# Kernel optimization log

Hardware: AMD Instinct MI355X
Metric: run time of the kernel (lower is better)

## Reference

```python
import jax, jax.numpy as jnp
import numpy as np

EMB = 1024
HEADS = 16
HEAD_DIM = EMB // HEADS
B, T = 2, 2048
EPS = 1e-5


def setup_inputs() -> dict:
    key = jax.random.key(0)
    ks = jax.random.split(key, 12)
    s_in = (1.0 / np.sqrt(EMB)).astype(np.float32)
    s_hid = (1.0 / np.sqrt(4 * EMB)).astype(np.float32)
    return {
        "x": jax.random.normal(ks[0], (B, T, EMB), jnp.float32),
        "Wq": jax.random.normal(ks[1], (HEADS, EMB, HEAD_DIM), jnp.float32) * s_in,
        "Wk": jax.random.normal(ks[2], (HEADS, EMB, HEAD_DIM), jnp.float32) * s_in,
        "Wv": jax.random.normal(ks[3], (HEADS, EMB, HEAD_DIM), jnp.float32) * s_in,
        "W1": jax.random.normal(ks[4], (EMB, 4 * EMB), jnp.float32) * s_in,
        "b1": jnp.zeros((4 * EMB,), jnp.float32),
        "W2": jax.random.normal(ks[5], (4 * EMB, EMB), jnp.float32) * s_hid,
        "b2": jnp.zeros((EMB,), jnp.float32),
        "g1": jnp.ones((EMB,), jnp.float32),
        "be1": jnp.zeros((EMB,), jnp.float32),
        "g2": jnp.ones((EMB,), jnp.float32),
        "be2": jnp.zeros((EMB,), jnp.float32),
    }


def _layernorm1d(x, gain, bias):
    # Faithful to source: normalize over dim 1 (sequence dim of [B,T,C]),
    # with UNBIASED variance (torch.var default).
    mean = jnp.mean(x, axis=1, keepdims=True)
    var = jnp.var(x, axis=1, keepdims=True, ddof=1)
    return gain * (x - mean) / jnp.sqrt(var + EPS) + bias


def _attention(x, Wq, Wk, Wv):
    Bq, Tq, C = x.shape
    q = jnp.einsum("btc,hcd->bhtd", x, Wq)
    k = jnp.einsum("btc,hcd->bhtd", x, Wk)
    v = jnp.einsum("btc,hcd->bhtd", x, Wv)
    # NOTE: scale uses input channel dim C (=emb_size), as in the source.
    wei = jnp.einsum("bhtd,bhsd->bhts", q, k) * (C ** -0.5)
    causal = jnp.tril(jnp.ones((Tq, Tq), bool))
    wei = jnp.where(causal, wei, -jnp.inf)
    wei = jax.nn.softmax(wei, axis=-1)
    out = jnp.einsum("bhts,bhsd->bhtd", wei, v)
    # concat over heads (dim=-1) == transpose + reshape
    return out.transpose(0, 2, 1, 3).reshape(Bq, Tq, -1)


def reference(x, Wq, Wk, Wv, W1, b1, W2, b2, g1, be1, g2, be2):
    x = x + _attention(_layernorm1d(x, g1, be1), Wq, Wk, Wv)
    h = _layernorm1d(x, g2, be2)
    h = jax.nn.relu(h @ W1 + b1) @ W2 + b2
    return x + h
```

## Files before the change

kernel.cpp:

```cpp
#include <hip/hip_runtime.h>


typedef __bf16 bf16x8 __attribute__((ext_vector_type(8)));
typedef float f32x4 __attribute__((ext_vector_type(4)));
typedef unsigned short u16;
typedef u16 u16x8 __attribute__((ext_vector_type(8)));
typedef u16 u16x4 __attribute__((ext_vector_type(4)));

#define MFMA16 __builtin_amdgcn_mfma_f32_16x16x32_bf16

__device__ __forceinline__ u16 f2bf(float f) {
  return __builtin_bit_cast(u16, (__bf16)f);
}
__device__ __forceinline__ float bf2f(u16 u) {
  return __builtin_bit_cast(float, (unsigned)u << 16);
}
__device__ __forceinline__ bf16x8 ldbf8(const u16* p) {
  return __builtin_bit_cast(bf16x8, *reinterpret_cast<const u16x8*>(p));
}
__device__ __forceinline__ void gll16(const void* g, void* l) {
  __builtin_amdgcn_global_load_lds((const __attribute__((address_space(1))) void*)g,
                                   (__attribute__((address_space(3))) void*)l, 16, 0, 0);
}
template <int N>
__device__ __forceinline__ void wait_vm() {
  if constexpr (N == 0)      asm volatile("s_waitcnt vmcnt(0)" ::: "memory");
  else if constexpr (N == 3) asm volatile("s_waitcnt vmcnt(3)" ::: "memory");
  else if constexpr (N == 4) asm volatile("s_waitcnt vmcnt(4)" ::: "memory");
  else                       asm volatile("s_waitcnt vmcnt(6)" ::: "memory");
}
__device__ __forceinline__ void barrier_raw() {
  asm volatile("" ::: "memory");
  __builtin_amdgcn_s_barrier();
  asm volatile("" ::: "memory");
}

__global__ __launch_bounds__(256) void transpose_big(const float* __restrict__ in,
                                                     u16* __restrict__ out, int K, int N) {
  __shared__ float tile[64][65];
  const int k0 = blockIdx.x * 64, n0 = blockIdx.y * 64;
  const int c = threadIdx.x & 63, rg = threadIdx.x >> 6;
#pragma unroll
  for (int i = 0; i < 16; ++i) {
    int r = rg * 16 + i;
    tile[r][c] = in[(size_t)(k0 + r) * N + n0 + c];
  }
  __syncthreads();
#pragma unroll
  for (int i = 0; i < 16; ++i) {
    int nl = rg * 16 + i;
    out[(size_t)(n0 + nl) * K + k0 + c] = f2bf(tile[c][nl]);
  }
}

__global__ __launch_bounds__(256) void transpose_head(const float* __restrict__ W,
                                                      u16* __restrict__ out, int zoff,
                                                      float scale) {
  __shared__ float tile[64][65];
  const int k0 = blockIdx.x * 64, h = blockIdx.y;
  const float* in = W + (size_t)h * 1024 * 64;
  const int c = threadIdx.x & 63, rg = threadIdx.x >> 6;
#pragma unroll
  for (int i = 0; i < 16; ++i) {
    int r = rg * 16 + i;
    tile[r][c] = in[(size_t)(k0 + r) * 64 + c];
  }
  __syncthreads();
#pragma unroll
  for (int i = 0; i < 16; ++i) {
    int nl = rg * 16 + i;
    out[(size_t)(zoff + h * 64 + nl) * 1024 + k0 + c] = f2bf(tile[c][nl] * scale);
  }
}

__global__ __launch_bounds__(256) void ln_partial(const float* __restrict__ x,
                                                  float2* __restrict__ part) {
  const int b = blockIdx.x >> 4, c0 = (blockIdx.x & 15) * 64;
  const int c = c0 + (threadIdx.x & 63), tg = threadIdx.x >> 6;
  const int t0 = blockIdx.y * 256 + tg * 64;
  float s = 0.f, sq = 0.f;
  const float* p = x + (size_t)(b * 2048 + t0) * 1024 + c;
#pragma unroll 8
  for (int i = 0; i < 64; ++i) {
    float v = p[(size_t)i * 1024];
    s += v; sq += v * v;
  }
  __shared__ float ss[256], sb[256];
  ss[threadIdx.x] = s; sb[threadIdx.x] = sq;
  __syncthreads();
  if (threadIdx.x < 64) {
    s  = ss[threadIdx.x] + ss[threadIdx.x + 64] + ss[threadIdx.x + 128] + ss[threadIdx.x + 192];
    sq = sb[threadIdx.x] + sb[threadIdx.x + 64] + sb[threadIdx.x + 128] + sb[threadIdx.x + 192];
    part[(size_t)(b * 1024 + c) * 8 + blockIdx.y] = make_float2(s, sq);
  }
}

__global__ __launch_bounds__(256) void ln_stats(const float2* __restrict__ part,
                                                float2* __restrict__ stats) {
  const int bc = blockIdx.x * 256 + threadIdx.x;
  float s = 0.f, sq = 0.f;
#pragma unroll
  for (int i = 0; i < 8; ++i) {
    float2 v = part[(size_t)bc * 8 + i];
    s += v.x; sq += v.y;
  }
  const float mean = s * (1.0f / 2048.0f);
  const float var = (sq - 2048.0f * mean * mean) * (1.0f / 2047.0f);
  stats[bc] = make_float2(mean, rsqrtf(var + 1e-5f));
}

__global__ __launch_bounds__(256) void ln_apply(const float* __restrict__ x,
                                                const float2* __restrict__ stats,
                                                const float* __restrict__ g,
                                                const float* __restrict__ be,
                                                u16* __restrict__ out) {
  const size_t flat = ((size_t)blockIdx.x * 256 + threadIdx.x) * 4;
  const int b = (int)(flat >> 21);
  const int c = (int)(flat & 1023);
  float4 xv = *reinterpret_cast<const float4*>(x + flat);
  float vs[4] = {xv.x, xv.y, xv.z, xv.w};
  u16x4 o;
#pragma unroll
  for (int j = 0; j < 4; ++j) {
    float2 st = stats[b * 1024 + c + j];
    o[j] = f2bf(g[c + j] * (vs[j] - st.x) * st.y + be[c + j]);
  }
  *reinterpret_cast<u16x4*>(out + flat) = o;
}

template <int WM, int WN, int EPI>
__global__ __launch_bounds__(512, 6) void gemm_kernel(const u16* __restrict__ A,
                                                      const u16* __restrict__ Bt,
                                                      u16* __restrict__ outb,
                                                      float* __restrict__ outf,
                                                      const float* __restrict__ bias,
                                                      const float* __restrict__ resid,
                                                      int N, int K) {
  constexpr int BM = WM * 32, BN = WN * 32;
  constexpr int ACH = BM / 8;
  constexpr int TC = (BM + BN) / 8;
  constexpr int LPW = TC / 8;
  static_assert(TC % 8 == 0, "chunks must divide evenly over 8 waves");
  __shared__ alignas(16) u16 sA[2][BM * 64];
  __shared__ alignas(16) u16 sB[2][BN * 64];
  const int gx = gridDim.x;
  const int nwg = gx * gridDim.y;
  int bid = blockIdx.y * gx + blockIdx.x;
  bid = (bid & 7) * (nwg >> 3) + (bid >> 3);
  const int n0 = (bid % gx) * BN, m0 = (bid / gx) * BM;
  const int tid = threadIdx.x, lane = tid & 63, wid = tid >> 6;
  const int wm = (wid / WN) * 32, wn = (wid % WN) * 32;
  const int lr = lane & 15, lg = lane >> 4;
  const int srow = lane >> 3;
  const int sgr = (lane & 7) ^ srow;
  const int x7 = lr & 7;
  f32x4 acc[2][2] = {};

  auto stage = [&](int buf, int k0) {
#pragma unroll
    for (int i = 0; i < LPW; ++i) {
      const int c = wid * LPW + i;
      if (c < ACH) {
        const int r = c * 8 + srow;
        gll16(A + (size_t)(m0 + r) * K + k0 + sgr * 8, &sA[buf][c * 512]);
      } else {
        const int r = (c - ACH) * 8 + srow;
        gll16(Bt + (size_t)(n0 + r) * K + k0 + sgr * 8, &sB[buf][(c - ACH) * 512]);
      }
    }
  };

  const int nsteps = K >> 6;
  stage(0, 0);
  int cur = 0;
  for (int t = 0; t < nsteps; ++t) {
    if (t + 1 < nsteps) {
      stage(cur ^ 1, (t + 1) * 64);
      wait_vm<LPW>();
    } else {
      wait_vm<0>();
    }
    barrier_raw();
    bf16x8 af[2][2], bfr[2][2];
#pragma unroll
    for (int mi = 0; mi < 2; ++mi)
#pragma unroll
      for (int kk = 0; kk < 2; ++kk)
        af[mi][kk] = ldbf8(&sA[cur][(wm + mi * 16 + lr) * 64 + (((kk * 4 + lg) ^ x7) * 8)]);
#pragma unroll
    for (int ni = 0; ni < 2; ++ni)
#pragma unroll
      for (int kk = 0; kk < 2; ++kk)
        bfr[ni][kk] = ldbf8(&sB[cur][(wn + ni * 16 + lr) * 64 + (((kk * 4 + lg) ^ x7) * 8)]);
#pragma unroll
    for (int kk = 0; kk < 2; ++kk)
#pragma unroll
      for (int mi = 0; mi < 2; ++mi)
#pragma unroll
        for (int ni = 0; ni < 2; ++ni)
          acc[mi][ni] = MFMA16(af[mi][kk], bfr[ni][kk], acc[mi][ni], 0, 0, 0);
    barrier_raw();
    cur ^= 1;
  }

#pragma unroll
  for (int mi = 0; mi < 2; ++mi)
#pragma unroll
    for (int ni = 0; ni < 2; ++ni)
#pragma unroll
      for (int r = 0; r < 4; ++r) {
        const int row = m0 + wm + mi * 16 + lg * 4 + r;
        const int col = n0 + wn + ni * 16 + lr;
        float v = acc[mi][ni][r];
        if (EPI == 0) {
          outb[(size_t)row * N + col] = f2bf(v);
        } else if (EPI == 1) {
          v += bias[col];
          v = fmaxf(v, 0.f);
          outb[(size_t)row * N + col] = f2bf(v);
        } else {
          v += bias[col] + resid[(size_t)row * N + col];
          outf[(size_t)row * N + col] = v;
        }
      }
}

__global__ __launch_bounds__(256) void attn_partial(const u16* __restrict__ qk,
                                                    const u16* __restrict__ vt,
                                                    u16* __restrict__ Opart,
                                                    float2* __restrict__ ml) {
  const int xr = 79 - (int)blockIdx.x;
  int qb, ch, nc;
  if (xr < 8)       { qb = xr;                ch = 0;            nc = 1; }
  else if (xr < 24) { qb = 8 + ((xr - 8) >> 1);  ch = (xr - 8) & 1;  nc = 2; }
  else if (xr < 48) { qb = 16 + (xr - 24) / 3;   ch = (xr - 24) % 3; nc = 3; }
  else              { qb = 24 + ((xr - 48) >> 2); ch = (xr - 48) & 3; nc = 4; }
  const int nt_tot = qb + 1;
  const int t0 = (ch * nt_tot) / nc;
  const int t1 = ((ch + 1) * nt_tot) / nc;
  const int bh = blockIdx.y, b = bh >> 4, h = bh & 15;
  const int slot = bh * 80 + xr;
  const int q0 = qb * 64;
  const int tid = threadIdx.x, lane = tid & 63, w = tid >> 6;
  const int lr = lane & 15, lg = lane >> 4;
  __shared__ alignas(16) u16 sK[2][64 * 64];
  __shared__ alignas(16) u16 sV[2][64 * 64];
  __shared__ alignas(16) u16 sP[4][16 * 64];

  const size_t qrow = (size_t)(b * 2048 + q0 + w * 16 + lr) * 2048 + h * 64;
  const bf16x8 aq0 = ldbf8(qk + qrow + lg * 8);
  const bf16x8 aq1 = ldbf8(qk + qrow + 32 + lg * 8);

  float m_i[4], l_i[4];
  f32x4 acc[4];
#pragma unroll
  for (int r = 0; r < 4; ++r) { m_i[r] = -1e30f; l_i[r] = 0.f; }
#pragma unroll
  for (int dn = 0; dn < 4; ++dn) acc[dn] = f32x4{0.f, 0.f, 0.f, 0.f};

  auto stage = [&](int buf, int s0) {
#pragma unroll
    for (int i = 0; i < 2; ++i) {
      const int c = w * 2 + i;
      const int g = c * 64 + lane;
      const int row = g >> 3;
      const int cs = (g & 7) ^ (row & 7);
      gll16(qk + (size_t)(b * 2048 + s0 + row) * 2048 + 1024 + h * 64 + cs * 8,
            &sK[buf][c * 512]);
      gll16(vt + (size_t)(h * 64 + row) * 4096 + b * 2048 + s0 + cs * 8,
            &sV[buf][c * 512]);
    }
  };

  stage(0, t0 * 64);

  for (int t = t0; t < t1; ++t) {
    const int buf = (t - t0) & 1;
    if (t + 1 < t1) {
      stage(buf ^ 1, (t + 1) * 64);
      wait_vm<4>();
    } else {
      wait_vm<0>();
    }
    barrier_raw();

    const u16* Kb = sK[buf];
    const u16* Vb = sV[buf];
    f32x4 sf[4];
    __builtin_amdgcn_s_setprio(1);
#pragma unroll
    for (int sn = 0; sn < 4; ++sn) {
      const int row = sn * 16 + lr;
      const int x7 = lr & 7;
      bf16x8 k0f = ldbf8(&Kb[row * 64 + ((lg ^ x7) * 8)]);
      bf16x8 k1f = ldbf8(&Kb[row * 64 + (((4 + lg) ^ x7) * 8)]);
      f32x4 z = {0.f, 0.f, 0.f, 0.f};
      z = MFMA16(aq0, k0f, z, 0, 0, 0);
      z = MFMA16(aq1, k1f, z, 0, 0, 0);
      sf[sn] = z;
    }
    __builtin_amdgcn_s_setprio(0);

    if (t == nt_tot - 1) {
      const int qlb = w * 16 + lg * 4;
#pragma unroll
      for (int sn = 0; sn < 4; ++sn)
#pragma unroll
        for (int r = 0; r < 4; ++r)
          if (sn * 16 + lr > qlb + r) sf[sn][r] = -1e30f;
    }

    float pm[4];
    bool need = false;
#pragma unroll
    for (int r = 0; r < 4; ++r) {
      pm[r] = fmaxf(fmaxf(sf[0][r], sf[1][r]), fmaxf(sf[2][r], sf[3][r]));
      need = need || (pm[r] > m_i[r] + 8.f);
    }
    if (__any(need)) {
#pragma unroll
      for (int r = 0; r < 4; ++r) {
        float mx = pm[r];
        mx = fmaxf(mx, __shfl_xor(mx, 1, 16));
        mx = fmaxf(mx, __shfl_xor(mx, 2, 16));
        mx = fmaxf(mx, __shfl_xor(mx, 4, 16));
        mx = fmaxf(mx, __shfl_xor(mx, 8, 16));
        const float mnew = fmaxf(m_i[r], mx);
        const float al = exp2f(m_i[r] - mnew);
        l_i[r] *= al;
        acc[0][r] *= al; acc[1][r] *= al; acc[2][r] *= al; acc[3][r] *= al;
        m_i[r] = mnew;
      }
    }

    const int x7p = lr & 7;
#pragma unroll
    for (int r = 0; r < 4; ++r) {
      const float p0 = exp2f(sf[0][r] - m_i[r]), p1 = exp2f(sf[1][r] - m_i[r]);
      const float p2 = exp2f(sf[2][r] - m_i[r]), p3 = exp2f(sf[3][r] - m_i[r]);
      l_i[r] += (p0 + p1) + (p2 + p3);
      const int prow = lg * 4 + r;
      const int pb = prow * 64, px = prow & 7;
      sP[w][pb + (((lr >> 3) ^ px) * 8) + (lr & 7)]       = f2bf(p0);
      sP[w][pb + (((2 + (lr >> 3)) ^ px) * 8) + (lr & 7)] = f2bf(p1);
      sP[w][pb + (((4 + (lr >> 3)) ^ px) * 8) + (lr & 7)] = f2bf(p2);
      sP[w][pb + (((6 + (lr >> 3)) ^ px) * 8) + (lr & 7)] = f2bf(p3);
    }

    const bf16x8 pa0 = ldbf8(&sP[w][lr * 64 + ((lg ^ x7p) * 8)]);
    const bf16x8 pa1 = ldbf8(&sP[w][lr * 64 + (((4 + lg) ^ x7p) * 8)]);
    __builtin_amdgcn_s_setprio(1);
#pragma unroll
    for (int dn = 0; dn < 4; ++dn) {
      const int row = dn * 16 + lr;
      bf16x8 v0f = ldbf8(&Vb[row * 64 + ((lg ^ x7p) * 8)]);
      bf16x8 v1f = ldbf8(&Vb[row * 64 + (((4 + lg) ^ x7p) * 8)]);
      acc[dn] = MFMA16(pa0, v0f, acc[dn], 0, 0, 0);
      acc[dn] = MFMA16(pa1, v1f, acc[dn], 0, 0, 0);
    }
    __builtin_amdgcn_s_setprio(0);
    barrier_raw();
  }

  const int rbase = w * 16 + lg * 4;
#pragma unroll
  for (int r = 0; r < 4; ++r) {
    float ls = l_i[r];
    ls += __shfl_xor(ls, 1, 16);
    ls += __shfl_xor(ls, 2, 16);
    ls += __shfl_xor(ls, 4, 16);
    ls += __shfl_xor(ls, 8, 16);
    const int row = rbase + r;
    if (lr == 0) ml[(size_t)slot * 64 + row] = make_float2(m_i[r], ls);
#pragma unroll
    for (int dn = 0; dn < 4; ++dn)
      Opart[((size_t)slot * 64 + row) * 64 + dn * 16 + lr] = f2bf(acc[dn][r]);
  }
}

__global__ __launch_bounds__(256) void attn_merge(const u16* __restrict__ Opart,
                                                  const float2* __restrict__ ml,
                                                  const float* __restrict__ x,
                                                  float* __restrict__ x2) {
  const int qb = blockIdx.x, bh = blockIdx.y, b = bh >> 4, h = bh & 15;
  int nc, s0;
  if (qb < 8)       { nc = 1; s0 = qb; }
  else if (qb < 16) { nc = 2; s0 = 8 + (qb - 8) * 2; }
  else if (qb < 24) { nc = 3; s0 = 24 + (qb - 16) * 3; }
  else              { nc = 4; s0 = 48 + (qb - 24) * 4; }
  const size_t slot0 = (size_t)bh * 80 + s0;
  const int tid = threadIdx.x;
  const int row = tid >> 2, d0 = (tid & 3) * 16;

  float wgt[4];
  float mmax = -1e30f, lsum = 0.f;
  for (int i = 0; i < nc; ++i) {
    float2 v = ml[(slot0 + i) * 64 + row];
    wgt[i] = v.x;
    mmax = fmaxf(mmax, v.x);
  }
  for (int i = 0; i < nc; ++i) {
    float2 v = ml[(slot0 + i) * 64 + row];
    wgt[i] = exp2f(wgt[i] - mmax);
    lsum += wgt[i] * v.y;
  }
  const float inv = 1.0f / lsum;

#pragma unroll
  for (int half = 0; half < 2; ++half) {
    const int d = d0 + half * 8;
    float o[8] = {0.f, 0.f, 0.f, 0.f, 0.f, 0.f, 0.f, 0.f};
    for (int i = 0; i < nc; ++i) {
      u16x8 v = *reinterpret_cast<const u16x8*>(&Opart[((slot0 + i) * 64 + row) * 64 + d]);
#pragma unroll
      for (int j = 0; j < 8; ++j) o[j] += wgt[i] * bf2f(v[j]);
    }
    const size_t idx = ((size_t)(b * 2048 + qb * 64 + row)) * 1024 + h * 64 + d;
    float4 x0 = *reinterpret_cast<const float4*>(x + idx);
    float4 x1 = *reinterpret_cast<const float4*>(x + idx + 4);
    float4 o0 = make_float4(x0.x + o[0] * inv, x0.y + o[1] * inv, x0.z + o[2] * inv, x0.w + o[3] * inv);
    float4 o1 = make_float4(x1.x + o[4] * inv, x1.y + o[5] * inv, x1.z + o[6] * inv, x1.w + o[7] * inv);
    *reinterpret_cast<float4*>(x2 + idx) = o0;
    *reinterpret_cast<float4*>(x2 + idx + 4) = o1;
  }
}

extern "C" void kernel_launch(void* const* d_in, const int* in_sizes, int n_in,
                              void* d_out, int out_size, void* d_ws, size_t ws_size,
                              hipStream_t stream) {
  const float* x   = (const float*)d_in[0];
  const float* Wq  = (const float*)d_in[1];
  const float* Wk  = (const float*)d_in[2];
  const float* Wv  = (const float*)d_in[3];
  const float* W1  = (const float*)d_in[4];
  const float* b1  = (const float*)d_in[5];
  const float* W2  = (const float*)d_in[6];
  const float* b2  = (const float*)d_in[7];
  const float* g1  = (const float*)d_in[8];
  const float* be1 = (const float*)d_in[9];
  const float* g2  = (const float*)d_in[10];
  const float* be2 = (const float*)d_in[11];
  float* out = (float*)d_out;

  char* ws = (char*)d_ws;
  size_t off = 0;
  auto alloc = [&](size_t bytes) { char* p = ws + off; off += (bytes + 255) & ~(size_t)255; return p; };
  u16*    qkb   = (u16*)alloc(4096ull * 2048 * 2);
  u16*    vtb   = (u16*)alloc(1024ull * 4096 * 2);
  (void)alloc(4096ull * 1024 * 2);
  u16*    h1    = qkb;
  float*  x2    = (float*)alloc(4096ull * 1024 * 4);
  u16*    hbuf  = (u16*)alloc(4096ull * 1024 * 2);
  u16*    wqkvt = (u16*)alloc(3072ull * 1024 * 2);
  u16*    w1t   = (u16*)alloc(4096ull * 1024 * 2);
  u16*    w2t   = (u16*)alloc(1024ull * 4096 * 2);
  float2* part  = (float2*)alloc(2048ull * 8 * 8);
  float2* stats = (float2*)alloc(2048ull * 8);
  u16*    Opart = (u16*)alloc(32ull * 80 * 64 * 64 * 2);
  float2* ml    = (float2*)alloc(32ull * 80 * 64 * 8);
  (void)ws_size; (void)in_sizes; (void)n_in; (void)out_size;

  const float SC = 0.03125f * 1.44269504088896341f;
  transpose_head<<<dim3(16, 16), 256, 0, stream>>>(Wq, wqkvt, 0, SC);
  transpose_head<<<dim3(16, 16), 256, 0, stream>>>(Wk, wqkvt, 1024, 1.0f);
  transpose_head<<<dim3(16, 16), 256, 0, stream>>>(Wv, wqkvt, 2048, 1.0f);
  transpose_big<<<dim3(16, 64), 256, 0, stream>>>(W1, w1t, 1024, 4096);
  transpose_big<<<dim3(64, 16), 256, 0, stream>>>(W2, w2t, 4096, 1024);

  ln_partial<<<dim3(32, 8), 256, 0, stream>>>(x, part);
  ln_stats<<<8, 256, 0, stream>>>(part, stats);
  ln_apply<<<4096, 256, 0, stream>>>(x, stats, g1, be1, hbuf);

  gemm_kernel<4, 2, 0><<<dim3(32, 32), 512, 0, stream>>>(hbuf, wqkvt, qkb, nullptr, nullptr, nullptr, 2048, 1024);
  gemm_kernel<2, 4, 0><<<dim3(32, 16), 512, 0, stream>>>(wqkvt + 2048 * 1024, hbuf, vtb, nullptr, nullptr, nullptr, 4096, 1024);

  attn_partial<<<dim3(80, 32), 256, 0, stream>>>(qkb, vtb, Opart, ml);
  attn_merge<<<dim3(32, 32), 256, 0, stream>>>(Opart, ml, x, x2);

  ln_partial<<<dim3(32, 8), 256, 0, stream>>>(x2, part);
  ln_stats<<<8, 256, 0, stream>>>(part, stats);
  ln_apply<<<4096, 256, 0, stream>>>(x2, stats, g2, be2, hbuf);

  gemm_kernel<4, 2, 1><<<dim3(64, 32), 512, 0, stream>>>(hbuf, w1t, h1, nullptr, b1, nullptr, 4096, 1024);

  gemm_kernel<4, 2, 2><<<dim3(16, 32), 512, 0, stream>>>(h1, w2t, nullptr, out, b2, x2, 1024, 4096);
}
```

Baseline: 269.9 us.

## Switch GEMMs to 128x128 tiles with 4 waves and 64x64 per-wave subtiles

Replaces the templated 8-wave GEMM (128x64 or 64x128 tiles, 32x32 per wave) with a fixed 128x128 block of 4 waves, each computing a 64x64 subtile with a 4x4 MFMA accumulator grid. Each wave now issues 8 global-to-LDS loads per k-step, and the wait count is adjusted to match. The aim is more register-level reuse and higher MFMA density per LDS read, so that LDS and global traffic per flop drop. In exchange it uses more registers, allows only 2 blocks per CU, and launches fewer blocks, for example only 256 for the W2 and V GEMMs.

```diff
diff --git a/kernel.cpp b/kernel.cpp
--- a/kernel.cpp
+++ b/kernel.cpp
@@ -25,9 +25,9 @@
 template <int N>
 __device__ __forceinline__ void wait_vm() {
   if constexpr (N == 0)      asm volatile("s_waitcnt vmcnt(0)" ::: "memory");
-  else if constexpr (N == 3) asm volatile("s_waitcnt vmcnt(3)" ::: "memory");
   else if constexpr (N == 4) asm volatile("s_waitcnt vmcnt(4)" ::: "memory");
-  else                       asm volatile("s_waitcnt vmcnt(6)" ::: "memory");
+  else if constexpr (N == 8) asm volatile("s_waitcnt vmcnt(8)" ::: "memory");
+  else                       asm volatile("s_waitcnt vmcnt(16)" ::: "memory");
 }
 __device__ __forceinline__ void barrier_raw() {
   asm volatile("" ::: "memory");
@@ -128,19 +128,15 @@
   *reinterpret_cast<u16x4*>(out + flat) = o;
 }
 
-template <int WM, int WN, int EPI>
-__global__ __launch_bounds__(512, 6) void gemm_kernel(const u16* __restrict__ A,
+template <int EPI>
+__global__ __launch_bounds__(256, 2) void gemm_kernel(const u16* __restrict__ A,
                                                       const u16* __restrict__ Bt,
                                                       u16* __restrict__ outb,
                                                       float* __restrict__ outf,
                                                       const float* __restrict__ bias,
                                                       const float* __restrict__ resid,
                                                       int N, int K) {
-  constexpr int BM = WM * 32, BN = WN * 32;
-  constexpr int ACH = BM / 8;
-  constexpr int TC = (BM + BN) / 8;
-  constexpr int LPW = TC / 8;
-  static_assert(TC % 8 == 0, "chunks must divide evenly over 8 waves");
+  constexpr int BM = 128, BN = 128;
   __shared__ alignas(16) u16 sA[2][BM * 64];
   __shared__ alignas(16) u16 sB[2][BN * 64];
   const int gx = gridDim.x;
@@ -149,23 +145,23 @@
   bid = (bid & 7) * (nwg >> 3) + (bid >> 3);
   const int n0 = (bid % gx) * BN, m0 = (bid / gx) * BM;
   const int tid = threadIdx.x, lane = tid & 63, wid = tid >> 6;
-  const int wm = (wid / WN) * 32, wn = (wid % WN) * 32;
+  const int wm = (wid >> 1) * 64, wn = (wid & 1) * 64;
   const int lr = lane & 15, lg = lane >> 4;
   const int srow = lane >> 3;
   const int sgr = (lane & 7) ^ srow;
   const int x7 = lr & 7;
-  f32x4 acc[2][2] = {};
+  f32x4 acc[4][4] = {};
 
   auto stage = [&](int buf, int k0) {
 #pragma unroll
-    for (int i = 0; i < LPW; ++i) {
-      const int c = wid * LPW + i;
-      if (c < ACH) {
+    for (int i = 0; i < 8; ++i) {
+      const int c = wid * 8 + i;
+      if (c < 16) {
         const int r = c * 8 + srow;
         gll16(A + (size_t)(m0 + r) * K + k0 + sgr * 8, &sA[buf][c * 512]);
       } else {
-        const int r = (c - ACH) * 8 + srow;
-        gll16(Bt + (size_t)(n0 + r) * K + k0 + sgr * 8, &sB[buf][(c - ACH) * 512]);
+        const int r = (c - 16) * 8 + srow;
+        gll16(Bt + (size_t)(n0 + r) * K + k0 + sgr * 8, &sB[buf][(c - 16) * 512]);
       }
     }
   };
@@ -176,37 +172,37 @@
   for (int t = 0; t < nsteps; ++t) {
     if (t + 1 < nsteps) {
       stage(cur ^ 1, (t + 1) * 64);
-      wait_vm<LPW>();
+      wait_vm<8>();
     } else {
       wait_vm<0>();
     }
     barrier_raw();
-    bf16x8 af[2][2], bfr[2][2];
-#pragma unroll
-    for (int mi = 0; mi < 2; ++mi)
+    bf16x8 af[4][2], bfr[4][2];
+#pragma unroll
+    for (int mi = 0; mi < 4; ++mi)
 #pragma unroll
       for (int kk = 0; kk < 2; ++kk)
         af[mi][kk] = ldbf8(&sA[cur][(wm + mi * 16 + lr) * 64 + (((kk * 4 + lg) ^ x7) * 8)]);
 #pragma unroll
-    for (int ni = 0; ni < 2; ++ni)
+    for (int ni = 0; ni < 4; ++ni)
 #pragma unroll
       for (int kk = 0; kk < 2; ++kk)
         bfr[ni][kk] = ldbf8(&sB[cur][(wn + ni * 16 + lr) * 64 + (((kk * 4 + lg) ^ x7) * 8)]);
 #pragma unroll
     for (int kk = 0; kk < 2; ++kk)
 #pragma unroll
-      for (int mi = 0; mi < 2; ++mi)
-#pragma unroll
-        for (int ni = 0; ni < 2; ++ni)
+      for (int mi = 0; mi < 4; ++mi)
+#pragma unroll
+        for (int ni = 0; ni < 4; ++ni)
           acc[mi][ni] = MFMA16(af[mi][kk], bfr[ni][kk], acc[mi][ni], 0, 0, 0);
     barrier_raw();
     cur ^= 1;
   }
 
 #pragma unroll
-  for (int mi = 0; mi < 2; ++mi)
-#pragma unroll
-    for (int ni = 0; ni < 2; ++ni)
+  for (int mi = 0; mi < 4; ++mi)
+#pragma unroll
+    for (int ni = 0; ni < 4; ++ni)
 #pragma unroll
       for (int r = 0; r < 4; ++r) {
         const int row = m0 + wm + mi * 16 + lg * 4 + r;
@@ -471,8 +467,8 @@
   ln_stats<<<8, 256, 0, stream>>>(part, stats);
   ln_apply<<<4096, 256, 0, stream>>>(x, stats, g1, be1, hbuf);
 
-  gemm_kernel<4, 2, 0><<<dim3(32, 32), 512, 0, stream>>>(hbuf, wqkvt, qkb, nullptr, nullptr, nullptr, 2048, 1024);
-  gemm_kernel<2, 4, 0><<<dim3(32, 16), 512, 0, stream>>>(wqkvt + 2048 * 1024, hbuf, vtb, nullptr, nullptr, nullptr, 4096, 1024);
+  gemm_kernel<0><<<dim3(16, 32), 256, 0, stream>>>(hbuf, wqkvt, qkb, nullptr, nullptr, nullptr, 2048, 1024);
+  gemm_kernel<0><<<dim3(32, 8), 256, 0, stream>>>(wqkvt + 2048 * 1024, hbuf, vtb, nullptr, nullptr, nullptr, 4096, 1024);
 
   attn_partial<<<dim3(80, 32), 256, 0, stream>>>(qkb, vtb, Opart, ml);
   attn_merge<<<dim3(32, 32), 256, 0, stream>>>(Opart, ml, x, x2);
@@ -481,7 +477,7 @@
   ln_stats<<<8, 256, 0, stream>>>(part, stats);
   ln_apply<<<4096, 256, 0, stream>>>(x2, stats, g2, be2, hbuf);
 
-  gemm_kernel<4, 2, 1><<<dim3(64, 32), 512, 0, stream>>>(hbuf, w1t, h1, nullptr, b1, nullptr, 4096, 1024);
-
-  gemm_kernel<4, 2, 2><<<dim3(16, 32), 512, 0, stream>>>(h1, w2t, nullptr, out, b2, x2, 1024, 4096);
-}
+  gemm_kernel<1><<<dim3(32, 32), 256, 0, stream>>>(hbuf, w1t, h1, nullptr, b1, nullptr, 4096, 1024);
+
+  gemm_kernel<2><<<dim3(8, 32), 256, 0, stream>>>(h1, w2t, nullptr, out, b2, x2, 1024, 4096);
+}
```

Result: faster. 255.0 us (-5.5%).
